# Optimization experiments

Hardware: AMD Instinct MI355X
Metric: run time of the kernel (lower is better)

The kernel has to match this reference:

```python
import jax, jax.numpy as jnp
import numpy as np

N, R, E = 100000, 3, 500000
IN_F, HID_F, OUT_F = 128, 128, 32


def setup_inputs() -> dict:
    key = jax.random.key(0)
    ks = jax.random.split(key, 12)
    inp = {
        "x": jax.random.normal(ks[0], (N, IN_F), dtype=jnp.float32),
        "src": jax.random.randint(ks[1], (R, E), 0, N, dtype=jnp.int32),
        "dst": jax.random.randint(ks[2], (R, E), 0, N, dtype=jnp.int32),
        # per-relation weights for the 4 layers (Glorot-ish scale)
        "W0": jax.random.normal(ks[3], (R, IN_F, HID_F), dtype=jnp.float32) / np.sqrt(IN_F),
        "b0": jnp.zeros((R, HID_F), dtype=jnp.float32),
        "W1": jax.random.normal(ks[4], (R, HID_F, HID_F), dtype=jnp.float32) / np.sqrt(HID_F),
        "b1": jnp.zeros((R, HID_F), dtype=jnp.float32),
        "W2": jax.random.normal(ks[5], (R, HID_F, HID_F), dtype=jnp.float32) / np.sqrt(HID_F),
        "b2": jnp.zeros((R, HID_F), dtype=jnp.float32),
        "W3": jax.random.normal(ks[6], (R, HID_F, OUT_F), dtype=jnp.float32) / np.sqrt(HID_F),
        "b3": jnp.zeros((R, OUT_F), dtype=jnp.float32),
    }
    return inp


def _degree_norms(src, dst, n_nodes):
    # DGL GraphConv norm='both': clamp degree to >=1, use deg^-1/2
    ones = jnp.ones(src.shape[1], dtype=jnp.float32)
    dout = jax.vmap(lambda s: jax.ops.segment_sum(ones, s, num_segments=n_nodes))(src)
    din = jax.vmap(lambda d: jax.ops.segment_sum(ones, d, num_segments=n_nodes))(dst)
    return jnp.clip(dout, 1.0) ** -0.5, jnp.clip(din, 1.0) ** -0.5  # [R, N] each


def _hetero_layer(h, W, b, src, dst, dout_is, din_is, relu):
    # per-relation GraphConv (norm='both'), HeteroGraphConv aggregate='sum'
    n = h.shape[0]
    out = None
    for r in range(W.shape[0]):
        hs = h * dout_is[r][:, None]                          # [N, d] scale src
        msg = hs[src[r]]                                       # [E, d] gather
        agg = jax.ops.segment_sum(msg, dst[r], num_segments=n) # [N, d] scatter-add
        agg = agg * din_is[r][:, None]
        o = agg @ W[r] + b[r]
        if relu:
            o = jax.nn.relu(o)  # activation inside GraphConv, before cross-rel sum
        out = o if out is None else out + o
    return out


def reference(x, src, dst, W0, b0, W1, b1, W2, b2, W3, b3):
    dout_is, din_is = _degree_norms(src, dst, x.shape[0])
    h = _hetero_layer(x, W0, b0, src, dst, dout_is, din_is, relu=True)
    h = _hetero_layer(h, W1, b1, src, dst, dout_is, din_is, relu=True)
    h = _hetero_layer(h, W2, b2, src, dst, dout_is, din_is, relu=True)
    h = _hetero_layer(h, W3, b3, src, dst, dout_is, din_is, relu=False)
    return h  # [N, OUT_F]
```

## Files before the change

### kernel.cpp

```cpp
#include <hip/hip_runtime.h>
#include <cstdint>
#include <cstddef>

#define NN 100000
#define RR 3
#define EE 500000
#define RN 300000
#define RE 1500000
#define KK 384
#define CAP 32

typedef unsigned short u16;
typedef unsigned int   u32;
typedef __attribute__((ext_vector_type(8))) short bhalf8;
typedef __attribute__((ext_vector_type(4))) float f32x4;
typedef __attribute__((ext_vector_type(4))) unsigned int u32x4;
typedef __attribute__((ext_vector_type(2))) unsigned int u32x2;

static inline int cdiv_h(int a, int b){ return (a+b-1)/b; }

__device__ __forceinline__ float bf_lo(u32 v){ union{u32 u; float f;} c; c.u = v<<16; return c.f; }
__device__ __forceinline__ float bf_hi(u32 v){ union{u32 u; float f;} c; c.u = v & 0xffff0000u; return c.f; }
__device__ __forceinline__ u16 f2bf(float f){
  union{float f; u32 u;} c; c.f = f;
  u32 r = (c.u + 0x7FFFu + ((c.u >> 16) & 1u)) >> 16;
  return (u16)r;
}
__device__ __forceinline__ u32 pk2(float a, float b){ return (u32)f2bf(a) | ((u32)f2bf(b)<<16); }
__device__ __forceinline__ float invdeg(int c){ return rsqrtf((float)(c > 1 ? c : 1)); }

__global__ __launch_bounds__(256) void k_init(int* __restrict__ cursor, int* __restrict__ dout_cnt){
  int i = blockIdx.x*256 + threadIdx.x;
  if (i < RN){ cursor[i] = i*CAP; dout_cnt[i] = 0; }
}

__global__ __launch_bounds__(256) void k_pre1f(const int* __restrict__ src, const int* __restrict__ dst,
    int* __restrict__ cursor, int* __restrict__ dout_cnt, int* __restrict__ edge_src,
    const float* __restrict__ x, u16* __restrict__ xb,
    const float* __restrict__ W0, const float* __restrict__ W1, const float* __restrict__ W2,
    const float* __restrict__ W3, u16* __restrict__ Wtb, u16* __restrict__ Wt3b){
  int b = blockIdx.x, t = threadIdx.x;
  if (b < 5860){
    int i = b*256 + t;
    if (i < RE){
      int r = i / EE;
      int s = src[i], d = dst[i];
      atomicAdd(&dout_cnt[r*NN + s], 1);
      int idx = r*NN + d;
      int pos = atomicAdd(&cursor[idx], 1);
      if (pos < idx*CAP + CAP) edge_src[pos] = s;
    }
  } else if (b < 12110){
    int i = (b-5860)*256 + t;
    if (i < NN*128/8){
      float4 v0 = ((const float4*)x)[i*2];
      float4 v1 = ((const float4*)x)[i*2+1];
      u32x4 o;
      o.x = pk2(v0.x, v0.y); o.y = pk2(v0.z, v0.w);
      o.z = pk2(v1.x, v1.y); o.w = pk2(v1.z, v1.w);
      __builtin_nontemporal_store(o, &((u32x4*)xb)[i]);
    }
  } else if (b < 12686){
    int gid = (b-12110)*256 + t;
    if (gid < 3*3*16384){
      int l = gid / 49152; int rem = gid - l*49152;
      int r = rem >> 14; int rem2 = rem & 16383;
      int k = rem2 >> 7; int n = rem2 & 127;
      const float* Wl = (l==0) ? W0 : (l==1) ? W1 : W2;
      __builtin_nontemporal_store(f2bf(Wl[rem]),
          &Wtb[((size_t)(l*3+r))*16384 + (size_t)n*128 + k]);
    }
  } else {
    int gid = (b-12686)*256 + t;
    if (gid < 3*4096){
      int r = gid >> 12; int rem = gid & 4095;
      int k = rem >> 5; int n = rem & 31;
      __builtin_nontemporal_store(f2bf(W3[gid]),
          &Wt3b[(size_t)(r*32+n)*128 + k]);
    }
  }
}

__global__ __launch_bounds__(256) void k_agg_bf(const u16* __restrict__ h, u16* __restrict__ AGG,
    const int* __restrict__ cursor, const int* __restrict__ edge_src,
    const int* __restrict__ dout_cnt){
  int w = (blockIdx.x*256 + threadIdx.x) >> 6;
  if (w >= RN) return;
  int l = threadIdx.x & 63;
  int q = l >> 4, k = l & 15;
  int r = w / NN;
  int n = w - r*NN;
  int s0 = w*CAP;
  int s1 = cursor[w];
  if (s1 > s0 + CAP) s1 = s0 + CAP;
  const int* __restrict__ dct = dout_cnt + r*NN;
  const u32x4* __restrict__ h4 = (const u32x4*)h;
  float a[8] = {0.f,0.f,0.f,0.f,0.f,0.f,0.f,0.f};
  for (int p = s0 + q; p < s1; p += 4){
    int s = edge_src[p];
    float wg = invdeg(dct[s]);
    u32x4 v = h4[(size_t)s*16 + k];
    a[0] += wg*bf_lo(v.x); a[1] += wg*bf_hi(v.x);
    a[2] += wg*bf_lo(v.y); a[3] += wg*bf_hi(v.y);
    a[4] += wg*bf_lo(v.z); a[5] += wg*bf_hi(v.z);
    a[6] += wg*bf_lo(v.w); a[7] += wg*bf_hi(v.w);
  }
  #pragma unroll
  for (int i=0;i<8;i++){
    a[i] += __shfl_xor(a[i], 16);
    a[i] += __shfl_xor(a[i], 32);
  }
  if (q == 0){
    float di = invdeg(s1 - s0);
    u32x4 o;
    o.x = pk2(a[0]*di, a[1]*di);
    o.y = pk2(a[2]*di, a[3]*di);
    o.z = pk2(a[4]*di, a[5]*di);
    o.w = pk2(a[6]*di, a[7]*di);
    __builtin_nontemporal_store(o, &((u32x4*)AGG)[(size_t)n*48 + r*16 + k]);
  }
}

__global__ __launch_bounds__(256) void k_mm_relu(const u16* __restrict__ A, const u16* __restrict__ Wt,
    const float* __restrict__ bias, u16* __restrict__ out){
  __shared__ __align__(16) u16 As[128*128];
  __shared__ __align__(16) u16 Bs[128*128];
  int t = threadIdx.x;
  int l = t & 63, w = t >> 6;
  int wr = w >> 1, wc = w & 1;
  int row0 = blockIdx.x * 128;
  int tr = t >> 4, tc = t & 15;
  int swz = tr & 7;

  int grow[8];
  #pragma unroll
  for (int it=0; it<8; ++it){
    int gr = row0 + it*16 + tr;
    grow[it] = gr > NN-1 ? NN-1 : gr;
  }

  f32x4 res[4][4];
  #pragma unroll
  for (int m=0;m<4;m++)
    #pragma unroll
    for (int n=0;n<4;n++) res[m][n] = (f32x4){0.f,0.f,0.f,0.f};

  u32x4 ra[8];
  #pragma unroll
  for (int it=0; it<8; ++it){
    ra[it] = __builtin_nontemporal_load((const u32x4*)&A[(size_t)grow[it]*KK + tc*8]);
    u32x4 rb = *(const u32x4*)&Wt[(size_t)(it*16 + tr)*128 + tc*8];
    *(u32x4*)&Bs[(it*16+tr)*128 + ((tc ^ swz)*8)] = rb;
  }
  #pragma unroll
  for (int it=0; it<8; ++it)
    *(u32x4*)&As[(it*16+tr)*128 + ((tc ^ swz)*8)] = ra[it];
  __syncthreads();

  for (int r=0; r<RR; r++){
    if (r+1 < RR){
      #pragma unroll
      for (int it=0; it<8; ++it)
        ra[it] = __builtin_nontemporal_load((const u32x4*)&A[(size_t)grow[it]*KK + (r+1)*128 + tc*8]);
    }

    f32x4 acc[4][4];
    #pragma unroll
    for (int m=0;m<4;m++)
      #pragma unroll
      for (int n=0;n<4;n++) acc[m][n] = (f32x4){0.f,0.f,0.f,0.f};

    #pragma unroll
    for (int kk=0; kk<4; ++kk){
      bhalf8 af[4], bf[4];
      #pragma unroll
      for (int m=0;m<4;m++){
        int rho = wr*64 + m*16 + (l&15);
        int ch = (kk*4 + (l>>4)) ^ (l&7);
        af[m] = *(const bhalf8*)&As[rho*128 + ch*8];
      }
      #pragma unroll
      for (int n=0;n<4;n++){
        int rho = wc*64 + n*16 + (l&15);
        int ch = (kk*4 + (l>>4)) ^ (l&7);
        bf[n] = *(const bhalf8*)&Bs[rho*128 + ch*8];
      }
      #pragma unroll
      for (int m=0;m<4;m++)
        #pragma unroll
        for (int n=0;n<4;n++)
          acc[m][n] = __builtin_amdgcn_mfma_f32_16x16x32_bf16(af[m], bf[n], acc[m][n], 0, 0, 0);
    }

    #pragma unroll
    for (int n=0;n<4;n++){
      int col = wc*64 + n*16 + (l&15);
      float bb = bias[r*128 + col];
      #pragma unroll
      for (int m=0;m<4;m++)
        #pragma unroll
        for (int i=0;i<4;i++){
          float v = acc[m][n][i] + bb;
          res[m][n][i] += v > 0.f ? v : 0.f;
        }
    }

    if (r+1 < RR){
      __syncthreads();
      #pragma unroll
      for (int it=0; it<8; ++it){
        u32x4 rb = *(const u32x4*)&Wt[(size_t)(r+1)*16384 + (size_t)(it*16 + tr)*128 + tc*8];
        *(u32x4*)&As[(it*16+tr)*128 + ((tc ^ swz)*8)] = ra[it];
        *(u32x4*)&Bs[(it*16+tr)*128 + ((tc ^ swz)*8)] = rb;
      }
      __syncthreads();
    }
  }

  #pragma unroll
  for (int m=0;m<4;m++)
    #pragma unroll
    for (int i=0;i<4;i++){
      int gr = row0 + wr*64 + m*16 + (l>>4)*4 + i;
      if (gr < NN){
        #pragma unroll
        for (int n=0;n<4;n++)
          out[(size_t)gr*128 + wc*64 + n*16 + (l&15)] = f2bf(res[m][n][i]);
      }
    }
}

__global__ __launch_bounds__(256) void k_mm_y(const u16* __restrict__ A, const u16* __restrict__ Wt3,
    u16* __restrict__ y){
  __shared__ __align__(16) u16 As[128*128];
  __shared__ __align__(16) u16 Bs[96*128];
  int t = threadIdx.x;
  int l = t & 63, w = t >> 6;
  int wr = w & 1, wc = w >> 1;
  int row0 = blockIdx.x * 128;
  int tr = t >> 4, tc = t & 15;
  int swz = tr & 7;

  u32x4 ra[8], rb[6];
  #pragma unroll
  for (int it=0; it<8; ++it){
    int grow = row0 + it*16 + tr;
    if (grow > NN-1) grow = NN-1;
    ra[it] = __builtin_nontemporal_load((const u32x4*)&A[(size_t)grow*128 + tc*8]);
  }
  #pragma unroll
  for (int it=0; it<6; ++it)
    rb[it] = *(const u32x4*)&Wt3[(size_t)(it*16 + tr)*128 + tc*8];
  #pragma unroll
  for (int it=0; it<8; ++it)
    *(u32x4*)&As[(it*16+tr)*128 + ((tc ^ swz)*8)] = ra[it];
  #pragma unroll
  for (int it=0; it<6; ++it)
    *(u32x4*)&Bs[(it*16+tr)*128 + ((tc ^ swz)*8)] = rb[it];
  __syncthreads();

  f32x4 acc[4][3];
  #pragma unroll
  for (int m=0;m<4;m++)
    #pragma unroll
    for (int n=0;n<3;n++) acc[m][n] = (f32x4){0.f,0.f,0.f,0.f};

  #pragma unroll
  for (int kk=0; kk<4; ++kk){
    bhalf8 af[4], bf[3];
    #pragma unroll
    for (int m=0;m<4;m++){
      int rho = wr*64 + m*16 + (l&15);
      int ch = (kk*4 + (l>>4)) ^ (l&7);
      af[m] = *(const bhalf8*)&As[rho*128 + ch*8];
    }
    #pragma unroll
    for (int n=0;n<3;n++){
      int rho = wc*48 + n*16 + (l&15);
      int ch = (kk*4 + (l>>4)) ^ (l&7);
      bf[n] = *(const bhalf8*)&Bs[rho*128 + ch*8];
    }
    #pragma unroll
    for (int m=0;m<4;m++)
      #pragma unroll
      for (int n=0;n<3;n++)
        acc[m][n] = __builtin_amdgcn_mfma_f32_16x16x32_bf16(af[m], bf[n], acc[m][n], 0, 0, 0);
  }

  #pragma unroll
  for (int m=0;m<4;m++)
    #pragma unroll
    for (int i=0;i<4;i++){
      int gr = row0 + wr*64 + m*16 + (l>>4)*4 + i;
      if (gr < NN){
        #pragma unroll
        for (int n=0;n<3;n++){
          int c = wc*48 + n*16 + (l&15);
          y[((size_t)(c>>5)*NN + gr)*32 + (c&31)] = f2bf(acc[m][n][i]);
        }
      }
    }
}

__global__ __launch_bounds__(256) void k_agg_out(const u16* __restrict__ y, float* __restrict__ out,
    const int* __restrict__ cursor, const int* __restrict__ edge_src,
    const int* __restrict__ dout_cnt, const float* __restrict__ b3){
  int n = (blockIdx.x*256 + threadIdx.x) >> 6;
  if (n >= NN) return;
  int l = threadIdx.x & 63;
  int g = l >> 3, k = l & 7;
  float res[4];
  #pragma unroll
  for (int i=0;i<4;i++) res[i] = b3[4*k+i] + b3[32+4*k+i] + b3[64+4*k+i];
  const u32x2* __restrict__ y2 = (const u32x2*)y;
  for (int r=0; r<RR; r++){
    int w = r*NN + n;
    int s0 = w*CAP;
    int s1 = cursor[w];
    if (s1 > s0 + CAP) s1 = s0 + CAP;
    const int* __restrict__ dct = dout_cnt + r*NN;
    float a[4] = {0.f,0.f,0.f,0.f};
    for (int p = s0 + g; p < s1; p += 8){
      int s = edge_src[p];
      float wg = invdeg(dct[s]);
      u32x2 v = y2[((size_t)r*NN + s)*8 + k];
      a[0] += wg*bf_lo(v.x); a[1] += wg*bf_hi(v.x);
      a[2] += wg*bf_lo(v.y); a[3] += wg*bf_hi(v.y);
    }
    #pragma unroll
    for (int i=0;i<4;i++){
      a[i] += __shfl_xor(a[i], 8);
      a[i] += __shfl_xor(a[i], 16);
      a[i] += __shfl_xor(a[i], 32);
    }
    float di = invdeg(s1 - s0);
    #pragma unroll
    for (int i=0;i<4;i++) res[i] += di*a[i];
  }
  if (g == 0)
    ((float4*)out)[(size_t)n*8 + k] = make_float4(res[0],res[1],res[2],res[3]);
}


extern "C" void kernel_launch(void* const* d_in, const int* in_sizes, int n_in,
                              void* d_out, int out_size, void* d_ws, size_t ws_size,
                              hipStream_t stream){
  const float* x   = (const float*)d_in[0];
  const int*   src = (const int*)d_in[1];
  const int*   dst = (const int*)d_in[2];
  const float* W0  = (const float*)d_in[3]; const float* b0 = (const float*)d_in[4];
  const float* W1  = (const float*)d_in[5]; const float* b1 = (const float*)d_in[6];
  const float* W2  = (const float*)d_in[7]; const float* b2 = (const float*)d_in[8];
  const float* W3  = (const float*)d_in[9]; const float* b3 = (const float*)d_in[10];
  float* out = (float*)d_out;

  char* p = (char*)d_ws;
  auto alloc = [&](size_t bytes)->char*{
    char* q = p; p += (bytes + 255) & ~(size_t)255; return q;
  };
  int*   cursor   = (int*)  alloc(RN*4);
  int*   dout_cnt = (int*)  alloc(RN*4);
  u16*   Wtb      = (u16*)  alloc((size_t)3*3*16384*2);
  u16*   Wt3b     = (u16*)  alloc((size_t)3*32*128*2);
  u16*   AGG      = (u16*)  alloc((size_t)NN*KK*2);
  u16*   bufA     = (u16*)  alloc((size_t)NN*128*2);
  u16*   bufB     = (u16*)  alloc((size_t)NN*128*2);
  int*   edge_src = (int*)  alloc((size_t)RN*CAP*4);
  u16*   y        = AGG;

  k_init <<<cdiv_h(RN,256),256,0,stream>>>(cursor, dout_cnt);
  k_pre1f<<<12734,256,0,stream>>>(src, dst, cursor, dout_cnt, edge_src,
                                  x, bufB, W0,W1,W2,W3, Wtb, Wt3b);

  int agg_blocks = cdiv_h(RN,4);
  int mm_blocks  = cdiv_h(NN,128);

  k_agg_bf<<<agg_blocks,256,0,stream>>>(bufB, AGG, cursor, edge_src, dout_cnt);
  k_mm_relu<<<mm_blocks,256,0,stream>>>(AGG, Wtb, b0, bufA);
  k_agg_bf<<<agg_blocks,256,0,stream>>>(bufA, AGG, cursor, edge_src, dout_cnt);
  k_mm_relu<<<mm_blocks,256,0,stream>>>(AGG, Wtb + 3*16384, b1, bufB);
  k_agg_bf<<<agg_blocks,256,0,stream>>>(bufB, AGG, cursor, edge_src, dout_cnt);
  k_mm_relu<<<mm_blocks,256,0,stream>>>(AGG, Wtb + 6*16384, b2, bufA);
  k_mm_y<<<mm_blocks,256,0,stream>>>(bufA, Wt3b, y);
  k_agg_out<<<cdiv_h(NN,4),256,0,stream>>>(y, out, cursor, edge_src, dout_cnt, b3);
}
```

Before: 656.7 us.

## Slice aggregation by feature column across blocks to improve gather cache locality

```diff
diff --git a/kernel.cpp b/kernel.cpp
--- a/kernel.cpp
+++ b/kernel.cpp
@@ -9,6 +9,7 @@
 #define RE 1500000
 #define KK 384
 #define CAP 32
+#define AGG_CHUNKS 4096
 
 typedef unsigned short u16;
 typedef unsigned int   u32;
@@ -81,43 +82,37 @@
   }
 }
 
-__global__ __launch_bounds__(256) void k_agg_bf(const u16* __restrict__ h, u16* __restrict__ AGG,
+__global__ __launch_bounds__(256) void k_agg_sl(const u16* __restrict__ h, u16* __restrict__ AGG,
     const int* __restrict__ cursor, const int* __restrict__ edge_src,
     const int* __restrict__ dout_cnt){
-  int w = (blockIdx.x*256 + threadIdx.x) >> 6;
-  if (w >= RN) return;
+  int slice = blockIdx.x & 7;
+  int chunk = blockIdx.x >> 3;
+  int wid = threadIdx.x >> 6;
   int l = threadIdx.x & 63;
-  int q = l >> 4, k = l & 15;
-  int r = w / NN;
-  int n = w - r*NN;
-  int s0 = w*CAP;
-  int s1 = cursor[w];
-  if (s1 > s0 + CAP) s1 = s0 + CAP;
-  const int* __restrict__ dct = dout_cnt + r*NN;
-  const u32x4* __restrict__ h4 = (const u32x4*)h;
-  float a[8] = {0.f,0.f,0.f,0.f,0.f,0.f,0.f,0.f};
-  for (int p = s0 + q; p < s1; p += 4){
-    int s = edge_src[p];
-    float wg = invdeg(dct[s]);
-    u32x4 v = h4[(size_t)s*16 + k];
-    a[0] += wg*bf_lo(v.x); a[1] += wg*bf_hi(v.x);
-    a[2] += wg*bf_lo(v.y); a[3] += wg*bf_hi(v.y);
-    a[4] += wg*bf_lo(v.z); a[5] += wg*bf_hi(v.z);
-    a[6] += wg*bf_lo(v.w); a[7] += wg*bf_hi(v.w);
-  }
-  #pragma unroll
-  for (int i=0;i<8;i++){
-    a[i] += __shfl_xor(a[i], 16);
-    a[i] += __shfl_xor(a[i], 32);
-  }
-  if (q == 0){
-    float di = invdeg(s1 - s0);
-    u32x4 o;
-    o.x = pk2(a[0]*di, a[1]*di);
-    o.y = pk2(a[2]*di, a[3]*di);
-    o.z = pk2(a[4]*di, a[5]*di);
-    o.w = pk2(a[6]*di, a[7]*di);
-    __builtin_nontemporal_store(o, &((u32x4*)AGG)[(size_t)n*48 + r*16 + k]);
+  int g = l >> 3, j = l & 7;
+  const u32* __restrict__ h32 = (const u32*)h;
+  u32* __restrict__ AGG32 = (u32*)AGG;
+  for (int w = chunk*4 + wid; w < RN; w += 4*AGG_CHUNKS){
+    int r = w / NN;
+    int n = w - r*NN;
+    int s0 = w*CAP;
+    int s1 = cursor[w];
+    if (s1 > s0 + CAP) s1 = s0 + CAP;
+    const int* __restrict__ dct = dout_cnt + r*NN;
+    float a0 = 0.f, a1 = 0.f;
+    for (int p = s0 + g; p < s1; p += 8){
+      int sE = edge_src[p];
+      float wg = invdeg(dct[sE]);
+      u32 v = h32[(size_t)sE*64 + slice*8 + j];
+      a0 += wg*bf_lo(v); a1 += wg*bf_hi(v);
+    }
+    a0 += __shfl_xor(a0, 8); a0 += __shfl_xor(a0, 16); a0 += __shfl_xor(a0, 32);
+    a1 += __shfl_xor(a1, 8); a1 += __shfl_xor(a1, 16); a1 += __shfl_xor(a1, 32);
+    if (g == 0){
+      float di = invdeg(s1 - s0);
+      __builtin_nontemporal_store(pk2(a0*di, a1*di),
+          &AGG32[(size_t)n*192 + r*64 + slice*8 + j]);
+    }
   }
 }
 
@@ -372,14 +367,14 @@
   k_pre1f<<<12734,256,0,stream>>>(src, dst, cursor, dout_cnt, edge_src,
                                   x, bufB, W0,W1,W2,W3, Wtb, Wt3b);
 
-  int agg_blocks = cdiv_h(RN,4);
-  int mm_blocks  = cdiv_h(NN,128);
-
-  k_agg_bf<<<agg_blocks,256,0,stream>>>(bufB, AGG, cursor, edge_src, dout_cnt);
+  int agg_grid = 8*AGG_CHUNKS;
+  int mm_blocks = cdiv_h(NN,128);
+
+  k_agg_sl<<<agg_grid,256,0,stream>>>(bufB, AGG, cursor, edge_src, dout_cnt);
   k_mm_relu<<<mm_blocks,256,0,stream>>>(AGG, Wtb, b0, bufA);
-  k_agg_bf<<<agg_blocks,256,0,stream>>>(bufA, AGG, cursor, edge_src, dout_cnt);
+  k_agg_sl<<<agg_grid,256,0,stream>>>(bufA, AGG, cursor, edge_src, dout_cnt);
   k_mm_relu<<<mm_blocks,256,0,stream>>>(AGG, Wtb + 3*16384, b1, bufB);
-  k_agg_bf<<<agg_blocks,256,0,stream>>>(bufB, AGG, cursor, edge_src, dout_cnt);
+  k_agg_sl<<<agg_grid,256,0,stream>>>(bufB, AGG, cursor, edge_src, dout_cnt);
   k_mm_relu<<<mm_blocks,256,0,stream>>>(AGG, Wtb + 6*16384, b2, bufA);
   k_mm_y<<<mm_blocks,256,0,stream>>>(bufA, Wt3b, y);
   k_agg_out<<<cdiv_h(NN,4),256,0,stream>>>(y, out, cursor, edge_src, dout_cnt, b3);
```

Result: slower. 1.559 ms (+137.5%).
